# Kernel tuning notes

Hardware: AMD Instinct MI355X
Metric: run time of the kernel (lower is better)

Reference implementation:

```python
import jax, jax.numpy as jnp
import numpy as np

B, N_ROWS, N_COLS, CTRL = 16384, 2048, 128, 1024
EPS = 1e-16


def setup_inputs() -> dict:
    key = jax.random.key(0)
    k1, k2, k3 = jax.random.split(key, 3)
    x = jax.random.normal(k1, (B, CTRL), dtype=jnp.float32)
    W_fc = jax.random.normal(k2, (CTRL, N_COLS + 6), dtype=jnp.float32) * 0.02
    b_fc = jnp.zeros((N_COLS + 6,), dtype=jnp.float32)
    M = jax.random.normal(k3, (N_ROWS, N_COLS), dtype=jnp.float32)
    # initial weighting: softmax of bias with w_bias[0]=100 -> ~one-hot at row 0
    w_bias = jnp.zeros((N_ROWS,), dtype=jnp.float32).at[0].set(100.0)
    w_prev = jnp.broadcast_to(jax.nn.softmax(w_bias), (B, N_ROWS))
    return {"x": x, "W_fc": W_fc, "b_fc": b_fc, "M": M, "w_prev": w_prev}


def reference(x, W_fc, b_fc, M, w_prev):
    # dense projection + split
    h = x @ W_fc + b_fc                      # [B, N_COLS+6]
    k = h[:, :N_COLS]                        # [B, N_COLS]
    beta = jax.nn.softplus(h[:, N_COLS:N_COLS + 1])          # [B, 1]
    g = jax.nn.sigmoid(h[:, N_COLS + 1:N_COLS + 2])          # [B, 1]
    s = jax.nn.softmax(h[:, N_COLS + 2:N_COLS + 5], axis=-1) # [B, 3]
    gamma = 1.0 + jax.nn.softplus(h[:, N_COLS + 5:N_COLS + 6])  # [B, 1]

    # content addressing: cosine similarity against every memory row
    k_norm = jnp.linalg.norm(k, axis=-1, keepdims=True)       # [B, 1]
    M_norm = jnp.linalg.norm(M, axis=-1)                      # [N_ROWS]
    sim = (k @ M.T) / (k_norm * M_norm[None, :] + EPS)        # [B, N_ROWS]
    w_c = jax.nn.softmax(beta * sim, axis=-1)

    # interpolation gate
    w_g = g * w_c + (1.0 - g) * w_prev

    # circular shift convolution (shifts -1, 0, +1)
    w_tilde = (s[:, 0:1] * jnp.roll(w_g, 1, axis=1)
               + s[:, 1:2] * w_g
               + s[:, 2:3] * jnp.roll(w_g, -1, axis=1))

    # sharpening
    w_pow = (w_tilde + EPS) ** gamma
    w = w_pow / jnp.sum(w_pow, axis=-1, keepdims=True)

    # weighted read
    r = w @ M                                                 # [B, N_COLS]
    return r
```

## Files before the change

kernel.cpp:

```cpp
#include <hip/hip_runtime.h>
#include <hip/hip_bf16.h>

#define NB    16384
#define NR    2048
#define NC    128
#define KCTRL 1024
#define EPSF  1e-16f
#define ESTR  2056
#define XSTR  1032

typedef __attribute__((ext_vector_type(8))) short bf16x8;
typedef __attribute__((ext_vector_type(4))) float f32x4;

__device__ __forceinline__ float softplus_f(float x) {
    return fmaxf(x, 0.f) + log1pf(__expf(-fabsf(x)));
}
__device__ __forceinline__ unsigned short f2bf(float f) {
    __hip_bfloat16 h = __float2bfloat16(f);
    return *(unsigned short*)&h;
}
__device__ __forceinline__ float bf2f(unsigned short u) {
    __hip_bfloat16 h;
    *(unsigned short*)&h = u;
    return __bfloat162float(h);
}

__device__ __forceinline__ size_t swz(int n, int k, int nch) {
    return ((size_t)((n >> 4) * nch + (k >> 5)) * 64 + ((k >> 3) & 3) * 16 + (n & 15)) * 8 + (k & 7);
}

__global__ __launch_bounds__(64) void prep_all(const float* __restrict__ M,
                                               unsigned short* __restrict__ Mb_sw,
                                               unsigned short* __restrict__ Mt_sw,
                                               float* __restrict__ imn,
                                               const float* __restrict__ W,
                                               unsigned short* __restrict__ Wt_sw) {
    const int bid = blockIdx.x;
    const int l = threadIdx.x;
    if (bid < NR) {
        const int i = bid;
        const float v0 = M[(size_t)i * NC + l];
        const float v1 = M[(size_t)i * NC + 64 + l];
        Mb_sw[swz(i, l, 4)]      = f2bf(v0);
        Mb_sw[swz(i, 64 + l, 4)] = f2bf(v1);
        Mt_sw[swz(l, i, 64)]      = f2bf(v0);
        Mt_sw[swz(64 + l, i, 64)] = f2bf(v1);
        float s = v0 * v0 + v1 * v1;
        #pragma unroll
        for (int m = 1; m < 64; m <<= 1) s += __shfl_xor(s, m);
        if (l == 0) imn[i] = 1.f / sqrtf(s);
    } else {
        const int k = bid - NR;
        Wt_sw[swz(l, k, 32)]      = f2bf(W[(size_t)k * 134 + l]);
        Wt_sw[swz(64 + l, k, 32)] = f2bf(W[(size_t)k * 134 + 64 + l]);
        if (l < 6) {
            Wt_sw[swz(128 + l, k, 32)] = f2bf(W[(size_t)k * 134 + 128 + l]);
        }
    }
}

__global__ __launch_bounds__(512, 4) void fused_ntm(const float* __restrict__ x,
                                                    const unsigned short* __restrict__ Wt_sw,
                                                    const float* __restrict__ bfc,
                                                    const unsigned short* __restrict__ Mb_sw,
                                                    const unsigned short* __restrict__ Mt_sw,
                                                    const float* __restrict__ imn,
                                                    const float* __restrict__ wprev,
                                                    float* __restrict__ out) {
    __shared__ __align__(16) unsigned short E_s[16][ESTR];
    __shared__ __align__(16) unsigned short k_s[16][136];
    __shared__ float h6s[16][6];
    __shared__ float ksum[16];
    __shared__ float scal_s[16][6];
    __shared__ float wred[16][8];
    __shared__ float fa_s[16], fc_s[16], invZ_s[16];

    unsigned short (*x_s)[XSTR] = (unsigned short(*)[XSTR])E_s;

    const int tid  = threadIdx.x;
    const int w    = tid >> 6;
    const int lane = tid & 63;
    const int quad = lane >> 4;
    const int l16  = lane & 15;
    const int b0   = blockIdx.x * 16;

    if (tid < 16) ksum[tid] = 0.f;

    #pragma unroll
    for (int p = 0; p < 8; p++) {
        const int idx = p * 512 + tid;
        const int row = idx >> 8;
        const int c4  = idx & 255;
        const float4 v = *(const float4*)(x + (size_t)(b0 + row) * KCTRL + c4 * 4);
        unsigned short* d = &x_s[row][c4 * 4];
        d[0] = f2bf(v.x); d[1] = f2bf(v.y); d[2] = f2bf(v.z); d[3] = f2bf(v.w);
    }
    __syncthreads();

    {
        f32x4 accF = {0.f, 0.f, 0.f, 0.f};
        f32x4 accH = {0.f, 0.f, 0.f, 0.f};
        const unsigned short* wbp = Wt_sw + (size_t)w * 16384 + lane * 8;
        const unsigned short* whp = Wt_sw + (size_t)8 * 16384 + lane * 8;
        bf16x8 bc0 = *(const bf16x8*)(wbp);
        bf16x8 bc1 = *(const bf16x8*)(wbp + 512);
        #pragma unroll
        for (int i = 0; i < 32; i += 2) {
            bf16x8 bn0, bn1;
            if (i < 30) {
                bn0 = *(const bf16x8*)(wbp + (size_t)(i + 2) * 512);
                bn1 = *(const bf16x8*)(wbp + (size_t)(i + 3) * 512);
            }
            const bf16x8 a0 = *(const bf16x8*)&x_s[l16][i * 32 + quad * 8];
            const bf16x8 a1 = *(const bf16x8*)&x_s[l16][(i + 1) * 32 + quad * 8];
            accF = __builtin_amdgcn_mfma_f32_16x16x32_bf16(a0, bc0, accF, 0, 0, 0);
            accF = __builtin_amdgcn_mfma_f32_16x16x32_bf16(a1, bc1, accF, 0, 0, 0);
            if (w == 0) {
                const bf16x8 h0 = *(const bf16x8*)(whp + (size_t)i * 512);
                const bf16x8 h1 = *(const bf16x8*)(whp + (size_t)(i + 1) * 512);
                accH = __builtin_amdgcn_mfma_f32_16x16x32_bf16(a0, h0, accH, 0, 0, 0);
                accH = __builtin_amdgcn_mfma_f32_16x16x32_bf16(a1, h1, accH, 0, 0, 0);
            }
            bc0 = bn0; bc1 = bn1;
        }
        __syncthreads();

        const float bb = bfc[w * 16 + l16];
        float part[4];
        #pragma unroll
        for (int reg = 0; reg < 4; reg++) {
            const int m = quad * 4 + reg;
            const float v = accF[reg] + bb;
            k_s[m][w * 16 + l16] = f2bf(v);
            part[reg] = v * v;
        }
        #pragma unroll
        for (int s = 1; s < 16; s <<= 1) {
            #pragma unroll
            for (int reg = 0; reg < 4; reg++) part[reg] += __shfl_xor(part[reg], s);
        }
        if (l16 == 0) {
            #pragma unroll
            for (int reg = 0; reg < 4; reg++) atomicAdd(&ksum[quad * 4 + reg], part[reg]);
        }
        if (w == 0 && l16 < 6) {
            const float bh = bfc[128 + l16];
            #pragma unroll
            for (int reg = 0; reg < 4; reg++) h6s[quad * 4 + reg][l16] = accH[reg] + bh;
        }
    }
    __syncthreads();

    if (tid < 16) {
        const float kn = sqrtf(ksum[tid]);
        const float* h = h6s[tid];
        const float beta = softplus_f(h[0]);
        const float g = 1.f / (1.f + __expf(-h[1]));
        const float m3 = fmaxf(h[2], fmaxf(h[3], h[4]));
        const float e0 = __expf(h[2] - m3), e1 = __expf(h[3] - m3), e2 = __expf(h[4] - m3);
        const float inv = 1.f / (e0 + e1 + e2);
        scal_s[tid][0] = beta / kn;
        scal_s[tid][1] = g;
        scal_s[tid][2] = e0 * inv;
        scal_s[tid][3] = e1 * inv;
        scal_s[tid][4] = e2 * inv;
        scal_s[tid][5] = 1.f + softplus_f(h[5]);
    }
    __syncthreads();

    {
        float cbs[4];
        #pragma unroll
        for (int reg = 0; reg < 4; reg++) cbs[reg] = scal_s[quad * 4 + reg][0];

        const bf16x8 af0 = *(const bf16x8*)&k_s[l16][quad * 8];
        const bf16x8 af1 = *(const bf16x8*)&k_s[l16][32 + quad * 8];
        const bf16x8 af2 = *(const bf16x8*)&k_s[l16][64 + quad * 8];
        const bf16x8 af3 = *(const bf16x8*)&k_s[l16][96 + quad * 8];

        const unsigned short* bpw = Mb_sw + (size_t)(w * 16) * 2048 + lane * 8;
        bf16x8 f00 = *(const bf16x8*)(bpw);
        bf16x8 f01 = *(const bf16x8*)(bpw + 512);
        bf16x8 f02 = *(const bf16x8*)(bpw + 1024);
        bf16x8 f03 = *(const bf16x8*)(bpw + 1536);
        bf16x8 f10 = *(const bf16x8*)(bpw + 2048);
        bf16x8 f11 = *(const bf16x8*)(bpw + 2048 + 512);
        bf16x8 f12 = *(const bf16x8*)(bpw + 2048 + 1024);
        bf16x8 f13 = *(const bf16x8*)(bpw + 2048 + 1536);
        float im0 = imn[(w * 16 + 0) * 16 + l16];
        float im1 = imn[(w * 16 + 1) * 16 + l16];

        float Sp[4] = {0.f, 0.f, 0.f, 0.f};
        #pragma unroll
        for (int t = 0; t < 16; t += 2) {
            {
                const int nt = w * 16 + t;
                f32x4 aA = {0.f, 0.f, 0.f, 0.f};
                f32x4 aB = {0.f, 0.f, 0.f, 0.f};
                aA = __builtin_amdgcn_mfma_f32_16x16x32_bf16(af0, f00, aA, 0, 0, 0);
                aB = __builtin_amdgcn_mfma_f32_16x16x32_bf16(af2, f02, aB, 0, 0, 0);
                aA = __builtin_amdgcn_mfma_f32_16x16x32_bf16(af1, f01, aA, 0, 0, 0);
                aB = __builtin_amdgcn_mfma_f32_16x16x32_bf16(af3, f03, aB, 0, 0, 0);
                const float imc = im0;
                if (t < 14) {
                    const unsigned short* bp = Mb_sw + (size_t)(nt + 2) * 2048 + lane * 8;
                    f00 = *(const bf16x8*)(bp);
                    f01 = *(const bf16x8*)(bp + 512);
                    f02 = *(const bf16x8*)(bp + 1024);
                    f03 = *(const bf16x8*)(bp + 1536);
                    im0 = imn[(nt + 2) * 16 + l16];
                }
                const int n0 = nt * 16;
                #pragma unroll
                for (int reg = 0; reg < 4; reg++) {
                    const float e = __expf((aA[reg] + aB[reg]) * cbs[reg] * imc);
                    E_s[quad * 4 + reg][n0 + l16] = f2bf(e);
                    Sp[reg] += e;
                }
            }
            {
                const int nt = w * 16 + t + 1;
                f32x4 aA = {0.f, 0.f, 0.f, 0.f};
                f32x4 aB = {0.f, 0.f, 0.f, 0.f};
                aA = __builtin_amdgcn_mfma_f32_16x16x32_bf16(af0, f10, aA, 0, 0, 0);
                aB = __builtin_amdgcn_mfma_f32_16x16x32_bf16(af2, f12, aB, 0, 0, 0);
                aA = __builtin_amdgcn_mfma_f32_16x16x32_bf16(af1, f11, aA, 0, 0, 0);
                aB = __builtin_amdgcn_mfma_f32_16x16x32_bf16(af3, f13, aB, 0, 0, 0);
                const float imc = im1;
                if (t < 13) {
                    const unsigned short* bp = Mb_sw + (size_t)(nt + 2) * 2048 + lane * 8;
                    f10 = *(const bf16x8*)(bp);
                    f11 = *(const bf16x8*)(bp + 512);
                    f12 = *(const bf16x8*)(bp + 1024);
                    f13 = *(const bf16x8*)(bp + 1536);
                    im1 = imn[(nt + 2) * 16 + l16];
                }
                const int n0 = nt * 16;
                #pragma unroll
                for (int reg = 0; reg < 4; reg++) {
                    const float e = __expf((aA[reg] + aB[reg]) * cbs[reg] * imc);
                    E_s[quad * 4 + reg][n0 + l16] = f2bf(e);
                    Sp[reg] += e;
                }
            }
        }
        #pragma unroll
        for (int s = 1; s < 16; s <<= 1) {
            #pragma unroll
            for (int reg = 0; reg < 4; reg++) Sp[reg] += __shfl_xor(Sp[reg], s);
        }
        if (l16 == 0) {
            #pragma unroll
            for (int reg = 0; reg < 4; reg++) wred[quad * 4 + reg][w] = Sp[reg];
        }
    }
    __syncthreads();
    if (tid < 16) {
        float S = 0.f;
        #pragma unroll
        for (int i = 0; i < 8; i++) S += wred[tid][i];
        const float g = scal_s[tid][1];
        fa_s[tid] = g / S;
        fc_s[tid] = 1.f - g;
    }
    __syncthreads();

    {
        const int row  = tid >> 5;
        const int g    = tid & 31;
        const int base = tid & 32;
        const float s0 = scal_s[row][2], s1 = scal_s[row][3], s2 = scal_s[row][4];
        const float gmm = scal_s[row][5];
        const float fa = fa_s[row], fcm = fc_s[row];
        const float* wp = wprev + (size_t)(b0 + row) * NR;

        int c0 = g * 8;
        bf16x8 E8c = *(const bf16x8*)&E_s[row][c0];
        float eLc  = bf2f(E_s[row][(c0 + NR - 1) & (NR - 1)]);
        float eRc  = bf2f(E_s[row][c0 + 8]);
        float4 wac = *(const float4*)(wp + c0);
        float4 wbc = *(const float4*)(wp + c0 + 4);
        float wpLc = wp[(c0 + NR - 1) & (NR - 1)];
        float wpRc = wp[c0 + 8];

        float Zp = 0.f, carry = 0.f, E0sav = 0.f;
        #pragma unroll
        for (int j = 0; j < 8; j++) {
            bf16x8 E8n; float eLn = 0.f, eRn = 0.f, wpLn = 0.f, wpRn = 0.f;
            float4 wan, wbn;
            if (j < 7) {
                const int c1 = c0 + 256;
                E8n  = *(const bf16x8*)&E_s[row][c1];
                eLn  = bf2f(E_s[row][c1 - 1]);
                eRn  = bf2f(E_s[row][(c1 + 8) & (NR - 1)]);
                wan  = *(const float4*)(wp + c1);
                wbn  = *(const float4*)(wp + c1 + 4);
                wpLn = wp[c1 - 1];
                wpRn = wp[(c1 + 8) & (NR - 1)];
            }
            float ef[8];
            #pragma unroll
            for (int i = 0; i < 8; i++) ef[i] = bf2f((unsigned short)E8c[i]);
            if (j == 0) E0sav = __shfl(ef[0], base);
            const float eL = (g == 0 && j > 0) ? carry : eLc;
            const float eR = (g == 31 && j == 7) ? E0sav : eRc;
            carry = __shfl(ef[7], base + 31);

            float wg[10];
            wg[0] = fmaf(fa, eL,    fcm * wpLc);
            wg[1] = fmaf(fa, ef[0], fcm * wac.x);
            wg[2] = fmaf(fa, ef[1], fcm * wac.y);
            wg[3] = fmaf(fa, ef[2], fcm * wac.z);
            wg[4] = fmaf(fa, ef[3], fcm * wac.w);
            wg[5] = fmaf(fa, ef[4], fcm * wbc.x);
            wg[6] = fmaf(fa, ef[5], fcm * wbc.y);
            wg[7] = fmaf(fa, ef[6], fcm * wbc.z);
            wg[8] = fmaf(fa, ef[7], fcm * wbc.w);
            wg[9] = fmaf(fa, eR,    fcm * wpRc);

            bf16x8 out8;
            #pragma unroll
            for (int i = 0; i < 8; i++) {
                const float wt = fmaf(s0, wg[i], fmaf(s1, wg[i + 1], s2 * wg[i + 2])) + EPSF;
                const float pw = exp2f(gmm * log2f(wt));
                Zp += pw;
                out8[i] = (short)f2bf(pw);
            }
            *(bf16x8*)&E_s[row][c0] = out8;

            c0 += 256;
            E8c = E8n; eLc = eLn; eRc = eRn;
            wac = wan; wbc = wbn; wpLc = wpLn; wpRc = wpRn;
        }
        #pragma unroll
        for (int s = 1; s < 32; s <<= 1) Zp += __shfl_xor(Zp, s);
        if (g == 0) invZ_s[row] = 1.f / Zp;
    }
    __syncthreads();

    {
        f32x4 acc0 = {0.f, 0.f, 0.f, 0.f};
        f32x4 acc1 = {0.f, 0.f, 0.f, 0.f};
        f32x4 acc2 = {0.f, 0.f, 0.f, 0.f};
        f32x4 acc3 = {0.f, 0.f, 0.f, 0.f};
        const unsigned short* bp = Mt_sw + (size_t)w * 32768 + lane * 8;
        bf16x8 c00 = *(const bf16x8*)(bp);
        bf16x8 c01 = *(const bf16x8*)(bp + 512);
        bf16x8 c02 = *(const bf16x8*)(bp + 1024);
        bf16x8 c03 = *(const bf16x8*)(bp + 1536);
        bf16x8 c10 = *(const bf16x8*)(bp + 2048);
        bf16x8 c11 = *(const bf16x8*)(bp + 2048 + 512);
        bf16x8 c12 = *(const bf16x8*)(bp + 2048 + 1024);
        bf16x8 c13 = *(const bf16x8*)(bp + 2048 + 1536);

        #pragma unroll
        for (int k0 = 0; k0 < NR; k0 += 256) {
            {
                const bf16x8 a0 = *(const bf16x8*)&E_s[l16][k0 + quad * 8];
                const bf16x8 a1 = *(const bf16x8*)&E_s[l16][k0 + 32 + quad * 8];
                const bf16x8 a2 = *(const bf16x8*)&E_s[l16][k0 + 64 + quad * 8];
                const bf16x8 a3 = *(const bf16x8*)&E_s[l16][k0 + 96 + quad * 8];
                acc0 = __builtin_amdgcn_mfma_f32_16x16x32_bf16(a0, c00, acc0, 0, 0, 0);
                acc1 = __builtin_amdgcn_mfma_f32_16x16x32_bf16(a1, c01, acc1, 0, 0, 0);
                acc2 = __builtin_amdgcn_mfma_f32_16x16x32_bf16(a2, c02, acc2, 0, 0, 0);
                acc3 = __builtin_amdgcn_mfma_f32_16x16x32_bf16(a3, c03, acc3, 0, 0, 0);
                if (k0 < NR - 256) {
                    const unsigned short* np = bp + (size_t)((k0 >> 5) + 8) * 512;
                    c00 = *(const bf16x8*)(np);
                    c01 = *(const bf16x8*)(np + 512);
                    c02 = *(const bf16x8*)(np + 1024);
                    c03 = *(const bf16x8*)(np + 1536);
                }
            }
            {
                const int k1 = k0 + 128;
                const bf16x8 a0 = *(const bf16x8*)&E_s[l16][k1 + quad * 8];
                const bf16x8 a1 = *(const bf16x8*)&E_s[l16][k1 + 32 + quad * 8];
                const bf16x8 a2 = *(const bf16x8*)&E_s[l16][k1 + 64 + quad * 8];
                const bf16x8 a3 = *(const bf16x8*)&E_s[l16][k1 + 96 + quad * 8];
                acc0 = __builtin_amdgcn_mfma_f32_16x16x32_bf16(a0, c10, acc0, 0, 0, 0);
                acc1 = __builtin_amdgcn_mfma_f32_16x16x32_bf16(a1, c11, acc1, 0, 0, 0);
                acc2 = __builtin_amdgcn_mfma_f32_16x16x32_bf16(a2, c12, acc2, 0, 0, 0);
                acc3 = __builtin_amdgcn_mfma_f32_16x16x32_bf16(a3, c13, acc3, 0, 0, 0);
                if (k0 < NR - 384) {
                    const unsigned short* np = bp + (size_t)((k0 >> 5) + 12) * 512;
                    c10 = *(const bf16x8*)(np);
                    c11 = *(const bf16x8*)(np + 512);
                    c12 = *(const bf16x8*)(np + 1024);
                    c13 = *(const bf16x8*)(np + 1536);
                }
            }
        }
        #pragma unroll
        for (int reg = 0; reg < 4; reg++) {
            const int m = quad * 4 + reg;
            const float v = (acc0[reg] + acc1[reg]) + (acc2[reg] + acc3[reg]);
            out[(size_t)(b0 + m) * NC + w * 16 + l16] = v * invZ_s[m];
        }
    }
}

extern "C" void kernel_launch(void* const* d_in, const int* in_sizes, int n_in,
                              void* d_out, int out_size, void* d_ws, size_t ws_size,
                              hipStream_t stream) {
    const float* x     = (const float*)d_in[0];
    const float* Wfc   = (const float*)d_in[1];
    const float* bfc   = (const float*)d_in[2];
    const float* M     = (const float*)d_in[3];
    const float* wprev = (const float*)d_in[4];
    float* out = (float*)d_out;

    char* ws = (char*)d_ws;
    float*          imn   = (float*)(ws);
    unsigned short* Mb_sw = (unsigned short*)(ws + 8192);
    unsigned short* Mt_sw = (unsigned short*)(ws + 532480);
    unsigned short* Wt_sw = (unsigned short*)(ws + 1056768);

    hipLaunchKernelGGL(prep_all, dim3(NR + KCTRL), dim3(64), 0, stream,
                       M, Mb_sw, Mt_sw, imn, Wfc, Wt_sw);
    hipLaunchKernelGGL(fused_ntm, dim3(NB / 16), dim3(512), 0, stream,
                       x, Wt_sw, bfc, Mb_sw, Mt_sw, imn, wprev, out);
}
```

Measured before the change: 290.5 us.

## Split fused NTM kernel into separate FC GEMM and head kernels

Pulls the dense projection out of the fused kernel into its own fc_gemm kernel. That kernel processes 32 rows per block, streams x in 128-column chunks through a small LDS tile, and writes k in bf16 plus the six per-row scalars to workspace. The head kernel then reads k and the scalars from global memory instead of computing them. The aim is to stop the large x staging buffer from sharing LDS with the addressing stage and to give the GEMM better weight reuse across 8 warps. In exchange it adds an extra launch and a global round trip for k, about 4MB.

```diff
diff --git a/kernel.cpp b/kernel.cpp
--- a/kernel.cpp
+++ b/kernel.cpp
@@ -1,13 +1,13 @@
 #include <hip/hip_runtime.h>
 #include <hip/hip_bf16.h>
 
-#define NB    16384
-#define NR    2048
-#define NC    128
-#define KCTRL 1024
-#define EPSF  1e-16f
-#define ESTR  2056
-#define XSTR  1032
+#define NB     16384
+#define NR     2048
+#define NC     128
+#define KCTRL  1024
+#define EPSF   1e-16f
+#define ESTR   2056
+#define R1ROWS 32
 
 typedef __attribute__((ext_vector_type(8))) short bf16x8;
 typedef __attribute__((ext_vector_type(4))) float f32x4;
@@ -59,99 +59,90 @@
     }
 }
 
-__global__ __launch_bounds__(512, 4) void fused_ntm(const float* __restrict__ x,
-                                                    const unsigned short* __restrict__ Wt_sw,
-                                                    const float* __restrict__ bfc,
-                                                    const unsigned short* __restrict__ Mb_sw,
-                                                    const unsigned short* __restrict__ Mt_sw,
-                                                    const float* __restrict__ imn,
-                                                    const float* __restrict__ wprev,
-                                                    float* __restrict__ out) {
-    __shared__ __align__(16) unsigned short E_s[16][ESTR];
-    __shared__ __align__(16) unsigned short k_s[16][136];
-    __shared__ float h6s[16][6];
-    __shared__ float ksum[16];
-    __shared__ float scal_s[16][6];
-    __shared__ float wred[16][8];
-    __shared__ float fa_s[16], fc_s[16], invZ_s[16];
-
-    unsigned short (*x_s)[XSTR] = (unsigned short(*)[XSTR])E_s;
+__global__ __launch_bounds__(512) void fc_gemm(const float* __restrict__ x,
+                                               const unsigned short* __restrict__ Wt_sw,
+                                               const float* __restrict__ bfc,
+                                               unsigned short* __restrict__ kb,
+                                               float* __restrict__ scal_g) {
+    __shared__ __align__(16) unsigned short x_s[R1ROWS][136];
+    __shared__ float ksum[R1ROWS];
+    __shared__ float h6s[R1ROWS][6];
 
     const int tid  = threadIdx.x;
     const int w    = tid >> 6;
     const int lane = tid & 63;
     const int quad = lane >> 4;
     const int l16  = lane & 15;
-    const int b0   = blockIdx.x * 16;
-
-    if (tid < 16) ksum[tid] = 0.f;
-
+    const int rg   = w >> 2;
+    const int cq   = w & 3;
+    const int b0   = blockIdx.x * R1ROWS;
+
+    if (tid < R1ROWS) ksum[tid] = 0.f;
+
+    f32x4 accA = {0.f, 0.f, 0.f, 0.f};
+    f32x4 accB = {0.f, 0.f, 0.f, 0.f};
+    f32x4 accH = {0.f, 0.f, 0.f, 0.f};
+    const unsigned short* wb = Wt_sw + lane * 8;
+    const size_t tA = (size_t)(cq * 2) * 32;
+    const size_t tB = (size_t)(cq * 2 + 1) * 32;
+    const size_t tH = (size_t)8 * 32;
+
+    for (int kc = 0; kc < 8; kc++) {
+        #pragma unroll
+        for (int p = 0; p < 2; p++) {
+            const int idx = p * 512 + tid;
+            const int row = idx >> 5;
+            const int c4  = idx & 31;
+            const float4 v = *(const float4*)(x + (size_t)(b0 + row) * KCTRL + kc * 128 + c4 * 4);
+            unsigned short* d = &x_s[row][c4 * 4];
+            d[0] = f2bf(v.x); d[1] = f2bf(v.y); d[2] = f2bf(v.z); d[3] = f2bf(v.w);
+        }
+        __syncthreads();
+        #pragma unroll
+        for (int ks = 0; ks < 4; ks++) {
+            const int sg = kc * 4 + ks;
+            const bf16x8 a  = *(const bf16x8*)&x_s[rg * 16 + l16][ks * 32 + quad * 8];
+            const bf16x8 bA = *(const bf16x8*)(wb + (tA + sg) * 512);
+            const bf16x8 bB = *(const bf16x8*)(wb + (tB + sg) * 512);
+            accA = __builtin_amdgcn_mfma_f32_16x16x32_bf16(a, bA, accA, 0, 0, 0);
+            accB = __builtin_amdgcn_mfma_f32_16x16x32_bf16(a, bB, accB, 0, 0, 0);
+            if (cq == 0) {
+                const bf16x8 bH = *(const bf16x8*)(wb + (tH + sg) * 512);
+                accH = __builtin_amdgcn_mfma_f32_16x16x32_bf16(a, bH, accH, 0, 0, 0);
+            }
+        }
+        __syncthreads();
+    }
+
+    float part[4];
     #pragma unroll
-    for (int p = 0; p < 8; p++) {
-        const int idx = p * 512 + tid;
-        const int row = idx >> 8;
-        const int c4  = idx & 255;
-        const float4 v = *(const float4*)(x + (size_t)(b0 + row) * KCTRL + c4 * 4);
-        unsigned short* d = &x_s[row][c4 * 4];
-        d[0] = f2bf(v.x); d[1] = f2bf(v.y); d[2] = f2bf(v.z); d[3] = f2bf(v.w);
+    for (int reg = 0; reg < 4; reg++) {
+        const int m = quad * 4 + reg;
+        const size_t grow = (size_t)(b0 + rg * 16 + m);
+        const float vA = accA[reg] + bfc[cq * 32 + l16];
+        const float vB = accB[reg] + bfc[cq * 32 + 16 + l16];
+        kb[grow * NC + cq * 32 + l16]      = f2bf(vA);
+        kb[grow * NC + cq * 32 + 16 + l16] = f2bf(vB);
+        part[reg] = vA * vA + vB * vB;
+    }
+    #pragma unroll
+    for (int s = 1; s < 16; s <<= 1) {
+        #pragma unroll
+        for (int reg = 0; reg < 4; reg++) part[reg] += __shfl_xor(part[reg], s);
+    }
+    if (l16 == 0) {
+        #pragma unroll
+        for (int reg = 0; reg < 4; reg++)
+            atomicAdd(&ksum[rg * 16 + quad * 4 + reg], part[reg]);
+    }
+    if (cq == 0 && l16 < 6) {
+        #pragma unroll
+        for (int reg = 0; reg < 4; reg++)
+            h6s[rg * 16 + quad * 4 + reg][l16] = accH[reg] + bfc[128 + l16];
     }
     __syncthreads();
 
-    {
-        f32x4 accF = {0.f, 0.f, 0.f, 0.f};
-        f32x4 accH = {0.f, 0.f, 0.f, 0.f};
-        const unsigned short* wbp = Wt_sw + (size_t)w * 16384 + lane * 8;
-        const unsigned short* whp = Wt_sw + (size_t)8 * 16384 + lane * 8;
-        bf16x8 bc0 = *(const bf16x8*)(wbp);
-        bf16x8 bc1 = *(const bf16x8*)(wbp + 512);
-        #pragma unroll
-        for (int i = 0; i < 32; i += 2) {
-            bf16x8 bn0, bn1;
-            if (i < 30) {
-                bn0 = *(const bf16x8*)(wbp + (size_t)(i + 2) * 512);
-                bn1 = *(const bf16x8*)(wbp + (size_t)(i + 3) * 512);
-            }
-            const bf16x8 a0 = *(const bf16x8*)&x_s[l16][i * 32 + quad * 8];
-            const bf16x8 a1 = *(const bf16x8*)&x_s[l16][(i + 1) * 32 + quad * 8];
-            accF = __builtin_amdgcn_mfma_f32_16x16x32_bf16(a0, bc0, accF, 0, 0, 0);
-            accF = __builtin_amdgcn_mfma_f32_16x16x32_bf16(a1, bc1, accF, 0, 0, 0);
-            if (w == 0) {
-                const bf16x8 h0 = *(const bf16x8*)(whp + (size_t)i * 512);
-                const bf16x8 h1 = *(const bf16x8*)(whp + (size_t)(i + 1) * 512);
-                accH = __builtin_amdgcn_mfma_f32_16x16x32_bf16(a0, h0, accH, 0, 0, 0);
-                accH = __builtin_amdgcn_mfma_f32_16x16x32_bf16(a1, h1, accH, 0, 0, 0);
-            }
-            bc0 = bn0; bc1 = bn1;
-        }
-        __syncthreads();
-
-        const float bb = bfc[w * 16 + l16];
-        float part[4];
-        #pragma unroll
-        for (int reg = 0; reg < 4; reg++) {
-            const int m = quad * 4 + reg;
-            const float v = accF[reg] + bb;
-            k_s[m][w * 16 + l16] = f2bf(v);
-            part[reg] = v * v;
-        }
-        #pragma unroll
-        for (int s = 1; s < 16; s <<= 1) {
-            #pragma unroll
-            for (int reg = 0; reg < 4; reg++) part[reg] += __shfl_xor(part[reg], s);
-        }
-        if (l16 == 0) {
-            #pragma unroll
-            for (int reg = 0; reg < 4; reg++) atomicAdd(&ksum[quad * 4 + reg], part[reg]);
-        }
-        if (w == 0 && l16 < 6) {
-            const float bh = bfc[128 + l16];
-            #pragma unroll
-            for (int reg = 0; reg < 4; reg++) h6s[quad * 4 + reg][l16] = accH[reg] + bh;
-        }
-    }
-    __syncthreads();
-
-    if (tid < 16) {
+    if (tid < R1ROWS) {
         const float kn = sqrtf(ksum[tid]);
         const float* h = h6s[tid];
         const float beta = softplus_f(h[0]);
@@ -159,12 +150,39 @@
         const float m3 = fmaxf(h[2], fmaxf(h[3], h[4]));
         const float e0 = __expf(h[2] - m3), e1 = __expf(h[3] - m3), e2 = __expf(h[4] - m3);
         const float inv = 1.f / (e0 + e1 + e2);
-        scal_s[tid][0] = beta / kn;
-        scal_s[tid][1] = g;
-        scal_s[tid][2] = e0 * inv;
-        scal_s[tid][3] = e1 * inv;
-        scal_s[tid][4] = e2 * inv;
-        scal_s[tid][5] = 1.f + softplus_f(h[5]);
+        float* sgp = scal_g + (size_t)(b0 + tid) * 6;
+        sgp[0] = beta / kn;
+        sgp[1] = g;
+        sgp[2] = e0 * inv;
+        sgp[3] = e1 * inv;
+        sgp[4] = e2 * inv;
+        sgp[5] = 1.f + softplus_f(h[5]);
+    }
+}
+
+__global__ __launch_bounds__(512, 4) void head_ntm(const unsigned short* __restrict__ kb,
+                                                   const float* __restrict__ scal_g,
+                                                   const unsigned short* __restrict__ Mb_sw,
+                                                   const unsigned short* __restrict__ Mt_sw,
+                                                   const float* __restrict__ imn,
+                                                   const float* __restrict__ wprev,
+                                                   float* __restrict__ out) {
+    __shared__ __align__(16) unsigned short E_s[16][ESTR];
+    __shared__ float scal_s[16][6];
+    __shared__ float wred[16][8];
+    __shared__ float fa_s[16], fc_s[16], invZ_s[16];
+
+    const int tid  = threadIdx.x;
+    const int w    = tid >> 6;
+    const int lane = tid & 63;
+    const int quad = lane >> 4;
+    const int l16  = lane & 15;
+    const int b0   = blockIdx.x * 16;
+
+    if (tid < 16) {
+        const float* sgp = scal_g + (size_t)(b0 + tid) * 6;
+        #pragma unroll
+        for (int j = 0; j < 6; j++) scal_s[tid][j] = sgp[j];
     }
     __syncthreads();
 
@@ -173,10 +191,11 @@
         #pragma unroll
         for (int reg = 0; reg < 4; reg++) cbs[reg] = scal_s[quad * 4 + reg][0];
 
-        const bf16x8 af0 = *(const bf16x8*)&k_s[l16][quad * 8];
-        const bf16x8 af1 = *(const bf16x8*)&k_s[l16][32 + quad * 8];
-        const bf16x8 af2 = *(const bf16x8*)&k_s[l16][64 + quad * 8];
-        const bf16x8 af3 = *(const bf16x8*)&k_s[l16][96 + quad * 8];
+        const unsigned short* kbp = kb + (size_t)(b0 + l16) * NC + quad * 8;
+        const bf16x8 af0 = *(const bf16x8*)(kbp);
+        const bf16x8 af1 = *(const bf16x8*)(kbp + 32);
+        const bf16x8 af2 = *(const bf16x8*)(kbp + 64);
+        const bf16x8 af3 = *(const bf16x8*)(kbp + 96);
 
         const unsigned short* bpw = Mb_sw + (size_t)(w * 16) * 2048 + lane * 8;
         bf16x8 f00 = *(const bf16x8*)(bpw);
@@ -411,13 +430,17 @@
     float* out = (float*)d_out;
 
     char* ws = (char*)d_ws;
-    float*          imn   = (float*)(ws);
-    unsigned short* Mb_sw = (unsigned short*)(ws + 8192);
-    unsigned short* Mt_sw = (unsigned short*)(ws + 532480);
-    unsigned short* Wt_sw = (unsigned short*)(ws + 1056768);
+    float*          imn    = (float*)(ws);
+    unsigned short* Mb_sw  = (unsigned short*)(ws + 8192);
+    unsigned short* Mt_sw  = (unsigned short*)(ws + 532480);
+    unsigned short* Wt_sw  = (unsigned short*)(ws + 1056768);
+    unsigned short* kb     = (unsigned short*)(ws + 1351680);
+    float*          scal_g = (float*)(ws + 5545984);
 
     hipLaunchKernelGGL(prep_all, dim3(NR + KCTRL), dim3(64), 0, stream,
                        M, Mb_sw, Mt_sw, imn, Wfc, Wt_sw);
-    hipLaunchKernelGGL(fused_ntm, dim3(NB / 16), dim3(512), 0, stream,
-                       x, Wt_sw, bfc, Mb_sw, Mt_sw, imn, wprev, out);
-}
+    hipLaunchKernelGGL(fc_gemm, dim3(NB / R1ROWS), dim3(512), 0, stream,
+                       x, Wt_sw, bfc, kb, scal_g);
+    hipLaunchKernelGGL(head_ntm, dim3(NB / 16), dim3(512), 0, stream,
+                       kb, scal_g, Mb_sw, Mt_sw, imn, wprev, out);
+}
```

Result: slower. 304.8 us (+4.9%).

## Double block to 1024 threads, splitting each phase across 16 waves

Applied to the files above, without the earlier changes.

Launches 16 waves per 16-row batch block instead of 8. The similarity phase gives each wave half as many memory-row tiles, the shift/sharpen phase maps one wave per batch row, and the read GEMM splits K into two halves, reduced through shared memory. The projection GEMM still uses only 8 waves. The aim is more latency hiding and parallelism per block, at the cost of extra syncs, idle waves in the projection phase, and register pressure under launch_bounds(1024, 8).

```diff
diff --git a/kernel.cpp b/kernel.cpp
--- a/kernel.cpp
+++ b/kernel.cpp
@@ -59,20 +59,20 @@
     }
 }
 
-__global__ __launch_bounds__(512, 4) void fused_ntm(const float* __restrict__ x,
-                                                    const unsigned short* __restrict__ Wt_sw,
-                                                    const float* __restrict__ bfc,
-                                                    const unsigned short* __restrict__ Mb_sw,
-                                                    const unsigned short* __restrict__ Mt_sw,
-                                                    const float* __restrict__ imn,
-                                                    const float* __restrict__ wprev,
-                                                    float* __restrict__ out) {
+__global__ __launch_bounds__(1024, 8) void fused_ntm(const float* __restrict__ x,
+                                                     const unsigned short* __restrict__ Wt_sw,
+                                                     const float* __restrict__ bfc,
+                                                     const unsigned short* __restrict__ Mb_sw,
+                                                     const unsigned short* __restrict__ Mt_sw,
+                                                     const float* __restrict__ imn,
+                                                     const float* __restrict__ wprev,
+                                                     float* __restrict__ out) {
     __shared__ __align__(16) unsigned short E_s[16][ESTR];
     __shared__ __align__(16) unsigned short k_s[16][136];
     __shared__ float h6s[16][6];
     __shared__ float ksum[16];
     __shared__ float scal_s[16][6];
-    __shared__ float wred[16][8];
+    __shared__ float wred[16][16];
     __shared__ float fa_s[16], fc_s[16], invZ_s[16];
 
     unsigned short (*x_s)[XSTR] = (unsigned short(*)[XSTR])E_s;
@@ -87,8 +87,8 @@
     if (tid < 16) ksum[tid] = 0.f;
 
     #pragma unroll
-    for (int p = 0; p < 8; p++) {
-        const int idx = p * 512 + tid;
+    for (int p = 0; p < 4; p++) {
+        const int idx = p * 1024 + tid;
         const int row = idx >> 8;
         const int c4  = idx & 255;
         const float4 v = *(const float4*)(x + (size_t)(b0 + row) * KCTRL + c4 * 4);
@@ -100,53 +100,57 @@
     {
         f32x4 accF = {0.f, 0.f, 0.f, 0.f};
         f32x4 accH = {0.f, 0.f, 0.f, 0.f};
-        const unsigned short* wbp = Wt_sw + (size_t)w * 16384 + lane * 8;
-        const unsigned short* whp = Wt_sw + (size_t)8 * 16384 + lane * 8;
-        bf16x8 bc0 = *(const bf16x8*)(wbp);
-        bf16x8 bc1 = *(const bf16x8*)(wbp + 512);
-        #pragma unroll
-        for (int i = 0; i < 32; i += 2) {
-            bf16x8 bn0, bn1;
-            if (i < 30) {
-                bn0 = *(const bf16x8*)(wbp + (size_t)(i + 2) * 512);
-                bn1 = *(const bf16x8*)(wbp + (size_t)(i + 3) * 512);
-            }
-            const bf16x8 a0 = *(const bf16x8*)&x_s[l16][i * 32 + quad * 8];
-            const bf16x8 a1 = *(const bf16x8*)&x_s[l16][(i + 1) * 32 + quad * 8];
-            accF = __builtin_amdgcn_mfma_f32_16x16x32_bf16(a0, bc0, accF, 0, 0, 0);
-            accF = __builtin_amdgcn_mfma_f32_16x16x32_bf16(a1, bc1, accF, 0, 0, 0);
-            if (w == 0) {
-                const bf16x8 h0 = *(const bf16x8*)(whp + (size_t)i * 512);
-                const bf16x8 h1 = *(const bf16x8*)(whp + (size_t)(i + 1) * 512);
-                accH = __builtin_amdgcn_mfma_f32_16x16x32_bf16(a0, h0, accH, 0, 0, 0);
-                accH = __builtin_amdgcn_mfma_f32_16x16x32_bf16(a1, h1, accH, 0, 0, 0);
-            }
-            bc0 = bn0; bc1 = bn1;
+        if (w < 8) {
+            const unsigned short* wbp = Wt_sw + (size_t)w * 16384 + lane * 8;
+            const unsigned short* whp = Wt_sw + (size_t)8 * 16384 + lane * 8;
+            bf16x8 bc0 = *(const bf16x8*)(wbp);
+            bf16x8 bc1 = *(const bf16x8*)(wbp + 512);
+            #pragma unroll
+            for (int i = 0; i < 32; i += 2) {
+                bf16x8 bn0, bn1;
+                if (i < 30) {
+                    bn0 = *(const bf16x8*)(wbp + (size_t)(i + 2) * 512);
+                    bn1 = *(const bf16x8*)(wbp + (size_t)(i + 3) * 512);
+                }
+                const bf16x8 a0 = *(const bf16x8*)&x_s[l16][i * 32 + quad * 8];
+                const bf16x8 a1 = *(const bf16x8*)&x_s[l16][(i + 1) * 32 + quad * 8];
+                accF = __builtin_amdgcn_mfma_f32_16x16x32_bf16(a0, bc0, accF, 0, 0, 0);
+                accF = __builtin_amdgcn_mfma_f32_16x16x32_bf16(a1, bc1, accF, 0, 0, 0);
+                if (w == 0) {
+                    const bf16x8 h0 = *(const bf16x8*)(whp + (size_t)i * 512);
+                    const bf16x8 h1 = *(const bf16x8*)(whp + (size_t)(i + 1) * 512);
+                    accH = __builtin_amdgcn_mfma_f32_16x16x32_bf16(a0, h0, accH, 0, 0, 0);
+                    accH = __builtin_amdgcn_mfma_f32_16x16x32_bf16(a1, h1, accH, 0, 0, 0);
+                }
+                bc0 = bn0; bc1 = bn1;
+            }
         }
         __syncthreads();
 
-        const float bb = bfc[w * 16 + l16];
-        float part[4];
-        #pragma unroll
-        for (int reg = 0; reg < 4; reg++) {
-            const int m = quad * 4 + reg;
-            const float v = accF[reg] + bb;
-            k_s[m][w * 16 + l16] = f2bf(v);
-            part[reg] = v * v;
-        }
-        #pragma unroll
-        for (int s = 1; s < 16; s <<= 1) {
-            #pragma unroll
-            for (int reg = 0; reg < 4; reg++) part[reg] += __shfl_xor(part[reg], s);
-        }
-        if (l16 == 0) {
-            #pragma unroll
-            for (int reg = 0; reg < 4; reg++) atomicAdd(&ksum[quad * 4 + reg], part[reg]);
-        }
-        if (w == 0 && l16 < 6) {
-            const float bh = bfc[128 + l16];
-            #pragma unroll
-            for (int reg = 0; reg < 4; reg++) h6s[quad * 4 + reg][l16] = accH[reg] + bh;
+        if (w < 8) {
+            const float bb = bfc[w * 16 + l16];
+            float part[4];
+            #pragma unroll
+            for (int reg = 0; reg < 4; reg++) {
+                const int m = quad * 4 + reg;
+                const float v = accF[reg] + bb;
+                k_s[m][w * 16 + l16] = f2bf(v);
+                part[reg] = v * v;
+            }
+            #pragma unroll
+            for (int s = 1; s < 16; s <<= 1) {
+                #pragma unroll
+                for (int reg = 0; reg < 4; reg++) part[reg] += __shfl_xor(part[reg], s);
+            }
+            if (l16 == 0) {
+                #pragma unroll
+                for (int reg = 0; reg < 4; reg++) atomicAdd(&ksum[quad * 4 + reg], part[reg]);
+            }
+            if (w == 0 && l16 < 6) {
+                const float bh = bfc[128 + l16];
+                #pragma unroll
+                for (int reg = 0; reg < 4; reg++) h6s[quad * 4 + reg][l16] = accH[reg] + bh;
+            }
         }
     }
     __syncthreads();
@@ -178,7 +182,7 @@
         const bf16x8 af2 = *(const bf16x8*)&k_s[l16][64 + quad * 8];
         const bf16x8 af3 = *(const bf16x8*)&k_s[l16][96 + quad * 8];
 
-        const unsigned short* bpw = Mb_sw + (size_t)(w * 16) * 2048 + lane * 8;
+        const unsigned short* bpw = Mb_sw + (size_t)(w * 8) * 2048 + lane * 8;
         bf16x8 f00 = *(const bf16x8*)(bpw);
         bf16x8 f01 = *(const bf16x8*)(bpw + 512);
         bf16x8 f02 = *(const bf16x8*)(bpw + 1024);
@@ -187,14 +191,14 @@
         bf16x8 f11 = *(const bf16x8*)(bpw + 2048 + 512);
         bf16x8 f12 = *(const bf16x8*)(bpw + 2048 + 1024);
         bf16x8 f13 = *(const bf16x8*)(bpw + 2048 + 1536);
-        float im0 = imn[(w * 16 + 0) * 16 + l16];
-        float im1 = imn[(w * 16 + 1) * 16 + l16];
+        float im0 = imn[(w * 8 + 0) * 16 + l16];
+        float im1 = imn[(w * 8 + 1) * 16 + l16];
 
         float Sp[4] = {0.f, 0.f, 0.f, 0.f};
         #pragma unroll
-        for (int t = 0; t < 16; t += 2) {
+        for (int t = 0; t < 8; t += 2) {
             {
-                const int nt = w * 16 + t;
+                const int nt = w * 8 + t;
                 f32x4 aA = {0.f, 0.f, 0.f, 0.f};
                 f32x4 aB = {0.f, 0.f, 0.f, 0.f};
                 aA = __builtin_amdgcn_mfma_f32_16x16x32_bf16(af0, f00, aA, 0, 0, 0);
@@ -202,7 +206,7 @@
                 aA = __builtin_amdgcn_mfma_f32_16x16x32_bf16(af1, f01, aA, 0, 0, 0);
                 aB = __builtin_amdgcn_mfma_f32_16x16x32_bf16(af3, f03, aB, 0, 0, 0);
                 const float imc = im0;
-                if (t < 14) {
+                if (t < 6) {
                     const unsigned short* bp = Mb_sw + (size_t)(nt + 2) * 2048 + lane * 8;
                     f00 = *(const bf16x8*)(bp);
                     f01 = *(const bf16x8*)(bp + 512);
@@ -219,7 +223,7 @@
                 }
             }
             {
-                const int nt = w * 16 + t + 1;
+                const int nt = w * 8 + t + 1;
                 f32x4 aA = {0.f, 0.f, 0.f, 0.f};
                 f32x4 aB = {0.f, 0.f, 0.f, 0.f};
                 aA = __builtin_amdgcn_mfma_f32_16x16x32_bf16(af0, f10, aA, 0, 0, 0);
@@ -227,7 +231,7 @@
                 aA = __builtin_amdgcn_mfma_f32_16x16x32_bf16(af1, f11, aA, 0, 0, 0);
                 aB = __builtin_amdgcn_mfma_f32_16x16x32_bf16(af3, f13, aB, 0, 0, 0);
                 const float imc = im1;
-                if (t < 13) {
+                if (t < 5) {
                     const unsigned short* bp = Mb_sw + (size_t)(nt + 2) * 2048 + lane * 8;
                     f10 = *(const bf16x8*)(bp);
                     f11 = *(const bf16x8*)(bp + 512);
@@ -258,7 +262,7 @@
     if (tid < 16) {
         float S = 0.f;
         #pragma unroll
-        for (int i = 0; i < 8; i++) S += wred[tid][i];
+        for (int i = 0; i < 16; i++) S += wred[tid][i];
         const float g = scal_s[tid][1];
         fa_s[tid] = g / S;
         fc_s[tid] = 1.f - g;
@@ -266,9 +270,8 @@
     __syncthreads();
 
     {
-        const int row  = tid >> 5;
-        const int g    = tid & 31;
-        const int base = tid & 32;
+        const int row = w;
+        const int g   = lane;
         const float s0 = scal_s[row][2], s1 = scal_s[row][3], s2 = scal_s[row][4];
         const float gmm = scal_s[row][5];
         const float fa = fa_s[row], fcm = fc_s[row];
@@ -285,11 +288,11 @@
 
         float Zp = 0.f, carry = 0.f, E0sav = 0.f;
         #pragma unroll
-        for (int j = 0; j < 8; j++) {
+        for (int j = 0; j < 4; j++) {
             bf16x8 E8n; float eLn = 0.f, eRn = 0.f, wpLn = 0.f, wpRn = 0.f;
             float4 wan, wbn;
-            if (j < 7) {
-                const int c1 = c0 + 256;
+            if (j < 3) {
+                const int c1 = c0 + 512;
                 E8n  = *(const bf16x8*)&E_s[row][c1];
                 eLn  = bf2f(E_s[row][c1 - 1]);
                 eRn  = bf2f(E_s[row][(c1 + 8) & (NR - 1)]);
@@ -301,10 +304,10 @@
             float ef[8];
             #pragma unroll
             for (int i = 0; i < 8; i++) ef[i] = bf2f((unsigned short)E8c[i]);
-            if (j == 0) E0sav = __shfl(ef[0], base);
+            if (j == 0) E0sav = __shfl(ef[0], 0);
             const float eL = (g == 0 && j > 0) ? carry : eLc;
-            const float eR = (g == 31 && j == 7) ? E0sav : eRc;
-            carry = __shfl(ef[7], base + 31);
+            const float eR = (g == 63 && j == 3) ? E0sav : eRc;
+            carry = __shfl(ef[7], 63);
 
             float wg[10];
             wg[0] = fmaf(fa, eL,    fcm * wpLc);
@@ -328,22 +331,25 @@
             }
             *(bf16x8*)&E_s[row][c0] = out8;
 
-            c0 += 256;
+            c0 += 512;
             E8c = E8n; eLc = eLn; eRc = eRn;
             wac = wan; wbc = wbn; wpLc = wpLn; wpRc = wpRn;
         }
         #pragma unroll
-        for (int s = 1; s < 32; s <<= 1) Zp += __shfl_xor(Zp, s);
+        for (int s = 1; s < 64; s <<= 1) Zp += __shfl_xor(Zp, s);
         if (g == 0) invZ_s[row] = 1.f / Zp;
     }
     __syncthreads();
 
     {
+        const int T  = w >> 1;
+        const int kh = w & 1;
+        const int kb = kh * 1024;
         f32x4 acc0 = {0.f, 0.f, 0.f, 0.f};
         f32x4 acc1 = {0.f, 0.f, 0.f, 0.f};
         f32x4 acc2 = {0.f, 0.f, 0.f, 0.f};
         f32x4 acc3 = {0.f, 0.f, 0.f, 0.f};
-        const unsigned short* bp = Mt_sw + (size_t)w * 32768 + lane * 8;
+        const unsigned short* bp = Mt_sw + (size_t)T * 32768 + (size_t)kh * 16384 + lane * 8;
         bf16x8 c00 = *(const bf16x8*)(bp);
         bf16x8 c01 = *(const bf16x8*)(bp + 512);
         bf16x8 c02 = *(const bf16x8*)(bp + 1024);
@@ -354,17 +360,18 @@
         bf16x8 c13 = *(const bf16x8*)(bp + 2048 + 1536);
 
         #pragma unroll
-        for (int k0 = 0; k0 < NR; k0 += 256) {
+        for (int k0 = 0; k0 < 1024; k0 += 256) {
             {
-                const bf16x8 a0 = *(const bf16x8*)&E_s[l16][k0 + quad * 8];
-                const bf16x8 a1 = *(const bf16x8*)&E_s[l16][k0 + 32 + quad * 8];
-                const bf16x8 a2 = *(const bf16x8*)&E_s[l16][k0 + 64 + quad * 8];
-                const bf16x8 a3 = *(const bf16x8*)&E_s[l16][k0 + 96 + quad * 8];
+                const int ka = kb + k0;
+                const bf16x8 a0 = *(const bf16x8*)&E_s[l16][ka + quad * 8];
+                const bf16x8 a1 = *(const bf16x8*)&E_s[l16][ka + 32 + quad * 8];
+                const bf16x8 a2 = *(const bf16x8*)&E_s[l16][ka + 64 + quad * 8];
+                const bf16x8 a3 = *(const bf16x8*)&E_s[l16][ka + 96 + quad * 8];
                 acc0 = __builtin_amdgcn_mfma_f32_16x16x32_bf16(a0, c00, acc0, 0, 0, 0);
                 acc1 = __builtin_amdgcn_mfma_f32_16x16x32_bf16(a1, c01, acc1, 0, 0, 0);
                 acc2 = __builtin_amdgcn_mfma_f32_16x16x32_bf16(a2, c02, acc2, 0, 0, 0);
                 acc3 = __builtin_amdgcn_mfma_f32_16x16x32_bf16(a3, c03, acc3, 0, 0, 0);
-                if (k0 < NR - 256) {
+                if (k0 < 1024 - 256) {
                     const unsigned short* np = bp + (size_t)((k0 >> 5) + 8) * 512;
                     c00 = *(const bf16x8*)(np);
                     c01 = *(const bf16x8*)(np + 512);
@@ -373,16 +380,16 @@
                 }
             }
             {
-                const int k1 = k0 + 128;
-                const bf16x8 a0 = *(const bf16x8*)&E_s[l16][k1 + quad * 8];
-                const bf16x8 a1 = *(const bf16x8*)&E_s[l16][k1 + 32 + quad * 8];
-                const bf16x8 a2 = *(const bf16x8*)&E_s[l16][k1 + 64 + quad * 8];
-                const bf16x8 a3 = *(const bf16x8*)&E_s[l16][k1 + 96 + quad * 8];
+                const int ka = kb + k0 + 128;
+                const bf16x8 a0 = *(const bf16x8*)&E_s[l16][ka + quad * 8];
+                const bf16x8 a1 = *(const bf16x8*)&E_s[l16][ka + 32 + quad * 8];
+                const bf16x8 a2 = *(const bf16x8*)&E_s[l16][ka + 64 + quad * 8];
+                const bf16x8 a3 = *(const bf16x8*)&E_s[l16][ka + 96 + quad * 8];
                 acc0 = __builtin_amdgcn_mfma_f32_16x16x32_bf16(a0, c10, acc0, 0, 0, 0);
                 acc1 = __builtin_amdgcn_mfma_f32_16x16x32_bf16(a1, c11, acc1, 0, 0, 0);
                 acc2 = __builtin_amdgcn_mfma_f32_16x16x32_bf16(a2, c12, acc2, 0, 0, 0);
                 acc3 = __builtin_amdgcn_mfma_f32_16x16x32_bf16(a3, c13, acc3, 0, 0, 0);
-                if (k0 < NR - 384) {
+                if (k0 < 1024 - 384) {
                     const unsigned short* np = bp + (size_t)((k0 >> 5) + 12) * 512;
                     c10 = *(const bf16x8*)(np);
                     c11 = *(const bf16x8*)(np + 512);
@@ -391,11 +398,25 @@
                 }
             }
         }
-        #pragma unroll
-        for (int reg = 0; reg < 4; reg++) {
-            const int m = quad * 4 + reg;
-            const float v = (acc0[reg] + acc1[reg]) + (acc2[reg] + acc3[reg]);
-            out[(size_t)(b0 + m) * NC + w * 16 + l16] = v * invZ_s[m];
+        __syncthreads();
+        float* pov = (float*)&E_s[0][0];
+        if (kh == 0) {
+            #pragma unroll
+            for (int reg = 0; reg < 4; reg++) {
+                const int m = quad * 4 + reg;
+                pov[((size_t)T * 16 + m) * 16 + l16] =
+                    (acc0[reg] + acc1[reg]) + (acc2[reg] + acc3[reg]);
+            }
+        }
+        __syncthreads();
+        if (kh == 1) {
+            #pragma unroll
+            for (int reg = 0; reg < 4; reg++) {
+                const int m = quad * 4 + reg;
+                const float v = pov[((size_t)T * 16 + m) * 16 + l16] +
+                                ((acc0[reg] + acc1[reg]) + (acc2[reg] + acc3[reg]));
+                out[(size_t)(b0 + m) * NC + T * 16 + l16] = v * invZ_s[m];
+            }
         }
     }
 }
@@ -418,6 +439,6 @@
 
     hipLaunchKernelGGL(prep_all, dim3(NR + KCTRL), dim3(64), 0, stream,
                        M, Mb_sw, Mt_sw, imn, Wfc, Wt_sw);
-    hipLaunchKernelGGL(fused_ntm, dim3(NB / 16), dim3(512), 0, stream,
+    hipLaunchKernelGGL(fused_ntm, dim3(NB / 16), dim3(1024), 0, stream,
                        x, Wt_sw, bfc, Mb_sw, Mt_sw, imn, wprev, out);
 }
```

New measurement: 314.2 us. +8.1%, slower.
